# Kernel tuning notes

Hardware: AMD Instinct MI355X
Metric: run time of the kernel (lower is better)

Reference implementation:

```python
import jax, jax.numpy as jnp
import numpy as np

NEG_SLOPE = 0.2
K_L = 0.5
K_G = 0.5
TEMP_G = 1e-3


def _leaky(v):
    return jnp.where(v >= 0, v, NEG_SLOPE * v)


def _topk_row_mask(scores, keep):
    # scores: [n, n, h]; torch.topk(dim=0) -> indices [keep, n] per head,
    # then head_mask[indices, :] = 1 selects whole ROWS (any column hit).
    n = scores.shape[0]
    s = jnp.transpose(scores, (1, 2, 0))        # [n_cols, h, n_rows]
    _, idx = jax.lax.top_k(s, keep)             # [n_cols, h, keep]

    def per_head(idx_h):                        # idx_h: [n_cols, keep]
        return jnp.zeros((n,), scores.dtype).at[idx_h.reshape(-1)].set(1.0)

    rows = jax.vmap(per_head, in_axes=1, out_axes=0)(idx)  # [h, n_rows]
    return jnp.transpose(rows)[:, None, :]      # [n_rows, 1, h] broadcast over cols


def setup_inputs() -> dict:
    key = jax.random.key(0)
    ks = jax.random.split(key, 8)
    n, in_f, feat_dim = 1024, 256, 128
    H, F = 4, 64                                # n_heads, n_hidden (out_features=256)
    feats = jax.random.normal(ks[0], (n, feat_dim), dtype=jnp.float32)
    x = jax.random.normal(ks[1], (n, in_f), dtype=jnp.float32)
    adj = jax.random.randint(ks[2], (n, n, 1), 0, 2).astype(jnp.int32)
    sc = 0.05
    W_l = jax.random.normal(ks[3], (in_f, H * F), dtype=jnp.float32) * sc
    W_r = jax.random.normal(ks[4], (in_f, H * F), dtype=jnp.float32) * sc
    attn_w = jax.random.normal(ks[5], (F,), dtype=jnp.float32) * sc
    W_delta = jax.random.normal(ks[6], (2 * F, F), dtype=jnp.float32) * sc
    b_delta = jnp.zeros((F,), dtype=jnp.float32)
    return {"feats": feats, "x": x, "adj": adj, "W_l": W_l, "W_r": W_r,
            "attn_w": attn_w, "W_delta": W_delta, "b_delta": b_delta}


def reference(feats, x, adj, W_l, W_r, attn_w, W_delta, b_delta):
    n = x.shape[0]
    F = attn_w.shape[0]
    H = W_l.shape[1] // F
    g_l = (x @ W_l).reshape(n, H, F)
    g_r = (x @ W_r).reshape(n, H, F)
    # g_sum[i, j] = g_l[j] + g_r[i]  (repeat vs repeat_interleave ordering)
    g_sum = g_r[:, None, :, :] + g_l[None, :, :, :]          # [n, n, H, F]
    e = jnp.einsum('ijhf,f->ijh', _leaky(g_sum), attn_w)     # [n, n, H]

    mask_adj = adj > 0                                        # [n, n, 1]
    a_l = jax.nn.softmax(jnp.where(mask_adj, e, -jnp.inf), axis=1)
    a_1nd = a_l * mask_adj.astype(e.dtype)

    keep_l = int(n * (1.0 - K_L))
    a_filt = a_1nd * _topk_row_mask(a_1nd, keep_l)
    attn_local = jnp.einsum('ijh,jhf->ihf', a_filt, g_r)     # [n, H, F]

    omega = jax.nn.softmax(e, axis=1)
    fn = (feats - feats.min(axis=0)) / (feats.max(axis=0) - feats.min(axis=0))
    fn = jnp.where(jnp.isnan(fn), 0.0, fn)
    g_rn = (g_r - g_r.min(axis=0)) / (g_r.max(axis=0) - g_r.min(axis=0))
    nf = jnp.linalg.norm(fn, axis=1)                          # [n] (index j)
    ng = jnp.linalg.norm(g_rn, axis=2)                        # [n, H] (index i)
    alpha = jax.nn.softmax(jnp.abs(nf[None, :, None] - ng[:, None, :]), axis=1)
    gamma = 0.5 * (omega + (1.0 - alpha))

    keep_g = int(n * (1.0 - K_G))
    gf = gamma * _topk_row_mask(gamma, keep_g)
    gf = jax.nn.softmax(jnp.where(gf == 0, 1e-10, gf) / TEMP_G, axis=1)
    attn_global = jnp.einsum('ijh,jhf->ihf', gf, g_r)         # [n, H, F]

    inter = _leaky(jnp.concatenate([attn_local, attn_global], axis=2) @ W_delta + b_delta)
    delta = jax.nn.softmax(inter, axis=1)                     # softmax over heads (torch dim=1)
    attn_res = delta * attn_local + (1.0 - delta) * attn_global
    return attn_res.reshape(n, H * F)
```

## Files before the change

kernel.cpp:

```cpp
#include <hip/hip_runtime.h>
#include <cstdint>
#include <cstddef>

#define N 1024
#define HN 4
#define FDIM 64
#define KSEL 512
#define FLT_MAX_ 3.402823466e+38f

__device__ __forceinline__ float wred_sum(float v){
#pragma unroll
  for(int o=32;o>0;o>>=1) v += __shfl_down(v,o,64);
  return v;
}
__device__ __forceinline__ float bfly_sum(float v){
#pragma unroll
  for(int o=1;o<64;o<<=1) v += __shfl_xor(v,o,64);
  return v;
}
__device__ __forceinline__ float bfly_max(float v){
#pragma unroll
  for(int o=1;o<64;o<<=1) v = fmaxf(v,__shfl_xor(v,o,64));
  return v;
}
__device__ __forceinline__ int bfly_sumi(int v){
#pragma unroll
  for(int o=1;o<64;o<<=1) v += __shfl_xor(v,o,64);
  return v;
}
__device__ __forceinline__ float bred_sum(float v, float* scr){
  int t=threadIdx.x;
  v = wred_sum(v);
  __syncthreads();
  if((t&63)==0) scr[t>>6]=v;
  __syncthreads();
  return (scr[0]+scr[1])+(scr[2]+scr[3]);
}

__global__ __launch_bounds__(256) void stage1(const float* __restrict__ x,
                                              const float* __restrict__ W_l,
                                              const float* __restrict__ W_r,
                                              const int* __restrict__ adj,
                                              float* __restrict__ g_l,
                                              float* __restrict__ g_r,
                                              unsigned* __restrict__ adjbit,
                                              int* __restrict__ masks){
  int bx = blockIdx.x, t = threadIdx.x;
  if(bx < 512){
    const float* __restrict__ W = (bx >= 256) ? W_r : W_l;
    float* __restrict__ g = (bx >= 256) ? g_r : g_l;
    int i0 = (bx & 255)*4;
    float acc[4] = {0.f,0.f,0.f,0.f};
#pragma unroll 8
    for(int k=0;k<256;k++){
      float w = W[(size_t)k*256 + t];
#pragma unroll
      for(int r=0;r<4;r++) acc[r] = fmaf(x[(size_t)(i0+r)*256 + k], w, acc[r]);
    }
#pragma unroll
    for(int r=0;r<4;r++) g[(size_t)(i0+r)*256 + t] = acc[r];
  } else {
    int i = bx - 512, w = t>>6, lane = t&63;
    if(i < 32) masks[i*256 + t] = 0;
#pragma unroll
    for(int it=0; it<4; it++){
      int j = w*256 + it*64 + lane;
      int v = adj[(size_t)i*N + j];
      unsigned long long mb = __ballot(v > 0);
      if(lane == 0){
        adjbit[i*32 + w*8 + it*2]     = (unsigned)mb;
        adjbit[i*32 + w*8 + it*2 + 1] = (unsigned)(mb >> 32);
      }
    }
  }
}

__global__ __launch_bounds__(256) void colmm_part(const float* __restrict__ feats,
                                                  const float* __restrict__ g_r,
                                                  float* __restrict__ pmin_f, float* __restrict__ pmax_f,
                                                  float* __restrict__ pmin_g, float* __restrict__ pmax_g){
  int bx = blockIdx.x, t = threadIdx.x;
  int src = (bx >= 16) ? 1 : 0;
  int chunk = src ? bx-16 : bx;
  int cols = src ? 256 : 128;
  const float* in = src ? g_r : feats;
  if(t < cols){
    float lo = FLT_MAX_, hi = -FLT_MAX_;
    int r0 = chunk*64;
    for(int r=0;r<64;r++){
      float v = in[(size_t)(r0+r)*cols + t];
      lo = fminf(lo,v); hi = fmaxf(hi,v);
    }
    if(src){ pmin_g[chunk*256+t]=lo; pmax_g[chunk*256+t]=hi; }
    else   { pmin_f[chunk*128+t]=lo; pmax_f[chunk*128+t]=hi; }
  }
}

__global__ __launch_bounds__(256) void norms_kernel(const float* __restrict__ feats,
                                                    const float* __restrict__ g_r,
                                                    const float* __restrict__ pmin_f, const float* __restrict__ pmax_f,
                                                    const float* __restrict__ pmin_g, const float* __restrict__ pmax_g,
                                                    float* __restrict__ nf, float* __restrict__ ng){
  __shared__ float scr[4];
  int i = blockIdx.x, z = blockIdx.y, t = threadIdx.x;
  if(z==0){
    float u = 0.f;
    if(t < 128){
      float lo = FLT_MAX_, hi = -FLT_MAX_;
#pragma unroll
      for(int k=0;k<16;k++){
        lo = fminf(lo, pmin_f[k*128+t]);
        hi = fmaxf(hi, pmax_f[k*128+t]);
      }
      float d = hi - lo;
      float v = feats[(size_t)i*128 + t];
      u = (d==0.f) ? 0.f : (v - lo)/d;
    }
    float tot = bred_sum(u*u, scr);
    if(t==0) nf[i] = sqrtf(tot);
  } else {
    int c = t, hh = t>>6;
    float lo = FLT_MAX_, hi = -FLT_MAX_;
#pragma unroll
    for(int k=0;k<16;k++){
      lo = fminf(lo, pmin_g[k*256+c]);
      hi = fmaxf(hi, pmax_g[k*256+c]);
    }
    float d = hi - lo;
    float v = g_r[(size_t)i*256 + c];
    float u = (v - lo)/d;
    float ss = wred_sum(u*u);
    if((t&63)==0) ng[hh*N + i] = sqrtf(ss);
  }
}

__global__ __launch_bounds__(256) void compute_e(const float* __restrict__ g_l,
                                                 const float* __restrict__ g_r,
                                                 const float* __restrict__ attn_w,
                                                 float* __restrict__ e){
  __shared__ __align__(16) float grs[64][68];
  __shared__ __align__(16) float gls[64][68];
  __shared__ __align__(16) float aw[64], aw2[64];
  int h = blockIdx.z, i0 = blockIdx.y*64, j0 = blockIdx.x*64;
  int t = threadIdx.x;
  if(t < 64){ float w = attn_w[t]; aw[t]=w; aw2[t]=0.2f*w; }
#pragma unroll
  for(int k=0;k<16;k++){
    int idx = t + k*256; int r = idx>>6, f = idx&63;
    grs[r][f] = g_r[(size_t)(i0+r)*256 + h*64 + f];
    gls[r][f] = g_l[(size_t)(j0+r)*256 + h*64 + f];
  }
  __syncthreads();
  int tj = t&15, ti = t>>4;
  float acc[4][4];
#pragma unroll
  for(int a=0;a<4;a++)
#pragma unroll
    for(int b=0;b<4;b++) acc[a][b]=0.f;
  for(int fc=0; fc<64; fc+=4){
    float4 wv  = *(float4*)&aw[fc];
    float4 wv2 = *(float4*)&aw2[fc];
    float4 ga4[4], gb4[4];
#pragma unroll
    for(int a=0;a<4;a++) ga4[a] = *(float4*)&grs[ti*4+a][fc];
#pragma unroll
    for(int b=0;b<4;b++) gb4[b] = *(float4*)&gls[tj+16*b][fc];
#pragma unroll
    for(int a=0;a<4;a++)
#pragma unroll
      for(int b=0;b<4;b++){
        float s0 = ga4[a].x + gb4[b].x;
        float s1 = ga4[a].y + gb4[b].y;
        float s2 = ga4[a].z + gb4[b].z;
        float s3 = ga4[a].w + gb4[b].w;
        acc[a][b] = fmaf(s0, (s0>=0.f)?wv.x:wv2.x, acc[a][b]);
        acc[a][b] = fmaf(s1, (s1>=0.f)?wv.y:wv2.y, acc[a][b]);
        acc[a][b] = fmaf(s2, (s2>=0.f)?wv.z:wv2.z, acc[a][b]);
        acc[a][b] = fmaf(s3, (s3>=0.f)?wv.w:wv2.w, acc[a][b]);
      }
  }
#pragma unroll
  for(int a=0;a<4;a++)
#pragma unroll
    for(int b=0;b<4;b++){
      int i = i0 + ti*4 + a, j = j0 + tj + 16*b;
      e[((size_t)h*N + i)*N + j] = acc[a][b];
    }
}

__global__ __launch_bounds__(256) void row_stats(const float* __restrict__ e,
                                                 const unsigned* __restrict__ adjbit,
                                                 const float* __restrict__ nf,
                                                 const float* __restrict__ ng,
                                                 float* __restrict__ mlA, float* __restrict__ islA,
                                                 float* __restrict__ moA, float* __restrict__ isoA,
                                                 float* __restrict__ maA, float* __restrict__ isaA,
                                                 float* __restrict__ mgA, float* __restrict__ sgA){
  int i = blockIdx.x, t = threadIdx.x, h = t>>6, lane = t&63;
  size_t base = ((size_t)h*N + i)*N;
  float er[16], nfr[16];
  unsigned nib[4];
#pragma unroll
  for(int c=0;c<4;c++){
    float4 e4 = *(const float4*)(e  + base + c*256 + lane*4);
    float4 n4 = *(const float4*)(nf + c*256 + lane*4);
    er[c*4+0]=e4.x; er[c*4+1]=e4.y; er[c*4+2]=e4.z; er[c*4+3]=e4.w;
    nfr[c*4+0]=n4.x; nfr[c*4+1]=n4.y; nfr[c*4+2]=n4.z; nfr[c*4+3]=n4.w;
    nib[c] = (adjbit[i*32 + c*8 + (lane>>3)] >> ((lane&7)*4)) & 0xFu;
  }
  float ngv = ng[h*N + i];
  float ml=-FLT_MAX_, mo=-FLT_MAX_, ma=-FLT_MAX_;
#pragma unroll
  for(int c=0;c<4;c++)
#pragma unroll
    for(int k=0;k<4;k++){
      int q = c*4+k;
      float ev = er[q];
      mo = fmaxf(mo, ev);
      if((nib[c]>>k)&1) ml = fmaxf(ml, ev);
      ma = fmaxf(ma, fabsf(nfr[q]-ngv));
    }
  ml = bfly_max(ml); mo = bfly_max(mo); ma = bfly_max(ma);
  float sl=0.f, so=0.f, sa=0.f;
#pragma unroll
  for(int c=0;c<4;c++)
#pragma unroll
    for(int k=0;k<4;k++){
      int q = c*4+k;
      float ev = er[q];
      so += __expf(ev-mo);
      if((nib[c]>>k)&1) sl += __expf(ev-ml);
      sa += __expf(fabsf(nfr[q]-ngv)-ma);
    }
  sl = bfly_sum(sl); so = bfly_sum(so); sa = bfly_sum(sa);
  float isl = 1.f/sl, iso = 1.f/so, isa = 1.f/sa;
  float gg[16];
  float mg = -FLT_MAX_;
#pragma unroll
  for(int q=0;q<16;q++){
    float ev = er[q];
    float omega = __expf(ev-mo)*iso;
    float alpha = __expf(fabsf(nfr[q]-ngv)-ma)*isa;
    float g = 0.5f*(omega + 1.f - alpha);
    gg[q] = g;
    mg = fmaxf(mg, g);
  }
  mg = bfly_max(mg);
  float sg = 0.f;
#pragma unroll
  for(int q=0;q<16;q++) sg += __expf((gg[q]-mg)/1e-3f);
  sg = bfly_sum(sg);
  if(lane==0){
    mlA[h*N+i]=ml; islA[h*N+i]=isl;
    moA[h*N+i]=mo; isoA[h*N+i]=iso;
    maA[h*N+i]=ma; isaA[h*N+i]=isa;
    mgA[h*N+i]=mg; sgA[h*N+i]=sg;
  }
}

__global__ __launch_bounds__(256) void applyT(float* __restrict__ e,
                                              float* __restrict__ gamT,
                                              const unsigned* __restrict__ adjbit,
                                              const float* __restrict__ nf,
                                              const float* __restrict__ mlA, const float* __restrict__ islA,
                                              const float* __restrict__ moA, const float* __restrict__ isoA,
                                              const float* __restrict__ maA, const float* __restrict__ isaA,
                                              const float* __restrict__ ng){
  __shared__ __align__(16) float buf1[64][65];
  __shared__ __align__(16) float buf2[64][65];
  __shared__ __align__(16) float buf3[64][65];
  __shared__ float rml[64], risl[64], rmo[64], riso[64], rma[64], risa[64], rng[64], nfs[64];
  int h = blockIdx.y;
  int pp = blockIdx.x; int a = 0;
  while(pp >= 16 - a){ pp -= 16 - a; a++; }
  int b = a + pp;
  int t = threadIdx.x;
  int rg = t >> 4, c4 = t & 15;

  int i0 = a*64, j0 = b*64;
  if(t < 64){
    int o = h*N + i0 + t;
    rml[t]=mlA[o]; risl[t]=islA[o]; rmo[t]=moA[o]; riso[t]=isoA[o];
    rma[t]=maA[o]; risa[t]=isaA[o]; rng[t]=ng[o]; nfs[t]=nf[j0+t];
  }
  __syncthreads();
  float4 ev[4]; unsigned nb[4];
#pragma unroll
  for(int k=0;k<4;k++){
    int row = rg*4+k;
    ev[k] = *(const float4*)(e + ((size_t)h*N + i0+row)*N + j0 + c4*4);
    nb[k] = (adjbit[(size_t)(i0+row)*32 + (j0>>5) + (c4>>3)] >> ((c4&7)*4)) & 0xFu;
  }
#pragma unroll
  for(int k=0;k<4;k++){
    int row = rg*4+k;
    float ml=rml[row], isl=risl[row], mo=rmo[row], iso=riso[row];
    float ma=rma[row], isa=risa[row], ngv=rng[row];
    float evc[4] = {ev[k].x,ev[k].y,ev[k].z,ev[k].w};
#pragma unroll
    for(int c=0;c<4;c++){
      int j = c4*4+c;
      buf2[j][row] = ((nb[k]>>c)&1) ? __expf(evc[c]-ml)*isl : 0.f;
      float omega = __expf(evc[c]-mo)*iso;
      float alpha = __expf(fabsf(nfs[j]-ngv)-ma)*isa;
      buf1[j][row] = 0.5f*(omega + 1.f - alpha);
    }
  }
  __syncthreads();
#pragma unroll
  for(int k=0;k<4;k++){
    int jr = rg*4+k;
    *(float4*)(gamT + ((size_t)h*N + j0+jr)*N + i0 + c4*4) = *(float4*)&buf1[jr][c4*4];
  }
  if(a == b){
#pragma unroll
    for(int k=0;k<4;k++){
      int jr = rg*4+k;
      *(float4*)(e + ((size_t)h*N + j0+jr)*N + i0 + c4*4) = *(float4*)&buf2[jr][c4*4];
    }
    return;
  }
  int i1 = b*64, j1 = a*64;
  __syncthreads();
  if(t < 64){
    int o = h*N + i1 + t;
    rml[t]=mlA[o]; risl[t]=islA[o]; rmo[t]=moA[o]; riso[t]=isoA[o];
    rma[t]=maA[o]; risa[t]=isaA[o]; rng[t]=ng[o]; nfs[t]=nf[j1+t];
  }
#pragma unroll
  for(int k=0;k<4;k++){
    int row = rg*4+k;
    ev[k] = *(const float4*)(e + ((size_t)h*N + i1+row)*N + j1 + c4*4);
    nb[k] = (adjbit[(size_t)(i1+row)*32 + (j1>>5) + (c4>>3)] >> ((c4&7)*4)) & 0xFu;
  }
  __syncthreads();
#pragma unroll
  for(int k=0;k<4;k++){
    int jr = rg*4+k;
    *(float4*)(e + ((size_t)h*N + i1+jr)*N + j1 + c4*4) = *(float4*)&buf2[jr][c4*4];
  }
#pragma unroll
  for(int k=0;k<4;k++){
    int row = rg*4+k;
    float ml=rml[row], isl=risl[row], mo=rmo[row], iso=riso[row];
    float ma=rma[row], isa=risa[row], ngv=rng[row];
    float evc[4] = {ev[k].x,ev[k].y,ev[k].z,ev[k].w};
#pragma unroll
    for(int c=0;c<4;c++){
      int j = c4*4+c;
      buf3[j][row] = ((nb[k]>>c)&1) ? __expf(evc[c]-ml)*isl : 0.f;
      float omega = __expf(evc[c]-mo)*iso;
      float alpha = __expf(fabsf(nfs[j]-ngv)-ma)*isa;
      buf1[j][row] = 0.5f*(omega + 1.f - alpha);
    }
  }
  __syncthreads();
#pragma unroll
  for(int k=0;k<4;k++){
    int jr = rg*4+k;
    *(float4*)(gamT + ((size_t)h*N + j1+jr)*N + i1 + c4*4) = *(float4*)&buf1[jr][c4*4];
    *(float4*)(e    + ((size_t)h*N + j1+jr)*N + i1 + c4*4) = *(float4*)&buf3[jr][c4*4];
  }
}

__global__ __launch_bounds__(256) void colselect6(const float* __restrict__ a1T,
                                                  const float* __restrict__ gaT,
                                                  int* __restrict__ mask_l,
                                                  int* __restrict__ mask_g){
  __shared__ __align__(16) int hist[4][256];
  int t = threadIdx.x, w = t>>6, lane = t&63;
  int gcol = blockIdx.x*4 + w;
  int z  = gcol >> 12;
  int hj = gcol & 4095;
  int h  = hj >> 10;
  const float* __restrict__ src = (z ? gaT : a1T) + (size_t)hj * (size_t)N;
  int* __restrict__ mask = z ? mask_g : mask_l;
  int* hw = hist[w];

  unsigned ur[16];
#pragma unroll
  for(int c=0;c<4;c++){
    uint4 u4 = ((const uint4*)src)[c*64 + lane];
    ur[c*4+0]=u4.x; ur[c*4+1]=u4.y; ur[c*4+2]=u4.z; ur[c*4+3]=u4.w;
  }
  int np = 0;
#pragma unroll
  for(int q=0;q<16;q++) np += (ur[q] != 0u) ? 1 : 0;
  int cnt_pos = bfly_sumi(np);

  unsigned T; int tneed; int tiecnt = -1;
  if(cnt_pos < KSEL){
    T = 0u; tneed = KSEL - cnt_pos;
  } else {
    unsigned prefix = 0; int kth = KSEL;
#pragma unroll
    for(int b=3;b>=0;b--){
      *(int4*)&hw[lane*4] = make_int4(0,0,0,0);
#pragma unroll
      for(int q=0;q<16;q++){
        unsigned u = ur[q];
        bool act = (b==3) || ((u >> (8*(b+1))) == prefix);
        if(act){
          int bucket = (u >> (8*b)) & 0xFF;
          unsigned long long mball = __ballot(true);
          int lead = __ffsll(mball) - 1;
          int maj = __shfl(bucket, lead, 64);
          if(bucket == maj){
            int cnt = (int)__popcll(__ballot(true));
            if(lane == lead) atomicAdd(&hw[maj], cnt);
          } else {
            atomicAdd(&hw[bucket], 1);
          }
        }
      }
      int4 hv = *(int4*)&hw[lane*4];
      int s = hv.x+hv.y+hv.z+hv.w;
      int P = s;
#pragma unroll
      for(int off=1; off<64; off<<=1){
        int q2 = __shfl_up(P, off, 64);
        if(lane >= off) P += q2;
      }
      int total = __shfl(P, 63, 64);
      int suffChunk  = total - (P - s);
      int suffChunkN = total - P;
      bool cross = (suffChunk >= kth) && (suffChunkN < kth);
      int selb=0, newk=0, tcnt=0;
      if(cross){
        int s3 = suffChunkN + hv.w;
        int s2 = s3 + hv.z;
        int s1 = s2 + hv.y;
        if(s3 >= kth){ selb=4*lane+3; newk = kth - suffChunkN; tcnt=hv.w; }
        else if(s2 >= kth){ selb=4*lane+2; newk = kth - s3; tcnt=hv.z; }
        else if(s1 >= kth){ selb=4*lane+1; newk = kth - s2; tcnt=hv.y; }
        else { selb=4*lane; newk = kth - s1; tcnt=hv.x; }
      }
      unsigned long long cm = __ballot(cross);
      int csrc = __ffsll(cm) - 1;
      selb   = __shfl(selb, csrc, 64);
      kth    = __shfl(newk, csrc, 64);
      tiecnt = __shfl(tcnt, csrc, 64);
      prefix = (prefix << 8) | (unsigned)selb;
    }
    T = prefix; tneed = kth;
  }

  if(tiecnt == tneed){
#pragma unroll
    for(int c=0;c<4;c++)
#pragma unroll
      for(int k2=0;k2<4;k2++){
        int i = c*256 + lane*4 + k2;
        if(ur[c*4+k2] >= T) mask[h*N + i] = 1;
      }
  } else {
    int base = 0;
#pragma unroll
    for(int c=0;c<4;c++){
      int tc=0;
#pragma unroll
      for(int k2=0;k2<4;k2++) tc += (ur[c*4+k2]==T)?1:0;
      int pc = tc;
#pragma unroll
      for(int off=1; off<64; off<<=1){
        int q2 = __shfl_up(pc, off, 64);
        if(lane >= off) pc += q2;
      }
      int ctot = __shfl(pc, 63, 64);
      int run = base + pc - tc;
#pragma unroll
      for(int k2=0;k2<4;k2++){
        int i = c*256 + lane*4 + k2;
        unsigned u = ur[c*4+k2];
        bool sel = (u > T) || (u == T && run < tneed);
        run += (u==T)?1:0;
        if(sel) mask[h*N + i] = 1;
      }
      base += ctot;
    }
  }
}

__global__ __launch_bounds__(256) void attn_mm(const float* __restrict__ a1T,
                                               const float* __restrict__ gaT,
                                               const float* __restrict__ g_r,
                                               const float* __restrict__ mgA,
                                               const float* __restrict__ sgA,
                                               const int* __restrict__ mask_g,
                                               float* __restrict__ partL,
                                               float* __restrict__ partG){
  __shared__ __align__(16) float a_t[32][36];
  __shared__ __align__(16) float p_t[32][36];
  __shared__ __align__(16) float b_s[32][68];
  __shared__ float mgv[32], isgv[32];
  __shared__ int mgf[32];
  int i0 = blockIdx.x*32, h = blockIdx.y, s = blockIdx.z, j0 = s*128;
  int t = threadIdx.x;
  if(t < 32){
    mgv[t]  = mgA[h*N + i0 + t];
    isgv[t] = 1.f / sgA[h*N + i0 + t];
    mgf[t]  = mask_g[h*N + i0 + t];
  }
  __syncthreads();
  int fq = t & 15, iq = t >> 4;
  float4 accL[2], accG[2];
#pragma unroll
  for(int r=0;r<2;r++){ accL[r]=make_float4(0,0,0,0); accG[r]=make_float4(0,0,0,0); }
  for(int sub=0; sub<4; sub++){
    int jb = j0 + sub*32;
    {
      int jj = t>>3, i4 = t&7;
      size_t base = ((size_t)h*N + jb + jj)*N + i0 + i4*4;
      *(float4*)&a_t[jj][i4*4] = *(const float4*)(a1T + base);
      float4 g4 = *(const float4*)(gaT + base);
      int ii = i4*4;
      const float inv = 1.f/1024.f;
      float4 p4;
      p4.x = mgf[ii+0] ? __expf((g4.x - mgv[ii+0])/1e-3f)*isgv[ii+0] : inv;
      p4.y = mgf[ii+1] ? __expf((g4.y - mgv[ii+1])/1e-3f)*isgv[ii+1] : inv;
      p4.z = mgf[ii+2] ? __expf((g4.z - mgv[ii+2])/1e-3f)*isgv[ii+2] : inv;
      p4.w = mgf[ii+3] ? __expf((g4.w - mgv[ii+3])/1e-3f)*isgv[ii+3] : inv;
      *(float4*)&p_t[jj][i4*4] = p4;
#pragma unroll
      for(int k=0;k<2;k++){
        int idx = t + k*256;
        int jb2 = idx>>4, d4 = idx&15;
        *(float4*)&b_s[jb2][d4*4] = *(const float4*)(g_r + (size_t)(jb+jb2)*256 + h*64 + d4*4);
      }
    }
    __syncthreads();
#pragma unroll 8
    for(int j=0;j<32;j++){
      float4 bv = *(float4*)&b_s[j][fq*4];
      float2 av = *(float2*)&a_t[j][iq*2];
      float2 pv = *(float2*)&p_t[j][iq*2];
      accL[0].x = fmaf(av.x, bv.x, accL[0].x); accL[0].y = fmaf(av.x, bv.y, accL[0].y);
      accL[0].z = fmaf(av.x, bv.z, accL[0].z); accL[0].w = fmaf(av.x, bv.w, accL[0].w);
      accL[1].x = fmaf(av.y, bv.x, accL[1].x); accL[1].y = fmaf(av.y, bv.y, accL[1].y);
      accL[1].z = fmaf(av.y, bv.z, accL[1].z); accL[1].w = fmaf(av.y, bv.w, accL[1].w);
      accG[0].x = fmaf(pv.x, bv.x, accG[0].x); accG[0].y = fmaf(pv.x, bv.y, accG[0].y);
      accG[0].z = fmaf(pv.x, bv.z, accG[0].z); accG[0].w = fmaf(pv.x, bv.w, accG[0].w);
      accG[1].x = fmaf(pv.y, bv.x, accG[1].x); accG[1].y = fmaf(pv.y, bv.y, accG[1].y);
      accG[1].z = fmaf(pv.y, bv.z, accG[1].z); accG[1].w = fmaf(pv.y, bv.w, accG[1].w);
    }
    __syncthreads();
  }
#pragma unroll
  for(int r=0;r<2;r++){
    int i = i0 + iq*2 + r;
    size_t o = ((size_t)s*N + i)*256 + h*64 + fq*4;
    *(float4*)&partL[o] = accL[r];
    *(float4*)&partG[o] = accG[r];
  }
}

__global__ __launch_bounds__(256) void epilogue(const float* __restrict__ partL,
                                                const float* __restrict__ partG,
                                                const int* __restrict__ mask_l,
                                                const float* __restrict__ W_delta,
                                                const float* __restrict__ b_delta,
                                                float* __restrict__ out){
  __shared__ float cat[4][128];
  __shared__ float inter_s[4][64];
  int i = blockIdx.x, t = threadIdx.x;
  int h = t>>6, f = t&63;
  float sl = 0.f, sg = 0.f;
#pragma unroll
  for(int s2=0;s2<8;s2++){
    size_t o = ((size_t)s2*N + i)*256 + h*64 + f;
    sl += partL[o];
    sg += partG[o];
  }
  if(!mask_l[h*N + i]) sl = 0.f;
  cat[h][f]      = sl;
  cat[h][64 + f] = sg;
  __syncthreads();
  float d = b_delta[f];
  for(int c=0;c<128;c++) d = fmaf(cat[h][c], W_delta[(size_t)c*64 + f], d);
  d = (d >= 0.f) ? d : 0.2f*d;
  inter_s[h][f] = d;
  __syncthreads();
  float m = inter_s[0][f];
#pragma unroll
  for(int hh=1;hh<4;hh++) m = fmaxf(m, inter_s[hh][f]);
  float ssum = 0.f;
#pragma unroll
  for(int hh=0;hh<4;hh++) ssum += __expf(inter_s[hh][f]-m);
  float delta = __expf(d - m)/ssum;
  out[(size_t)i*256 + h*64 + f] = delta*sl + (1.f - delta)*sg;
}

extern "C" void kernel_launch(void* const* d_in, const int* in_sizes, int n_in,
                              void* d_out, int out_size, void* d_ws, size_t ws_size,
                              hipStream_t stream) {
  const float* feats  = (const float*)d_in[0];
  const float* x      = (const float*)d_in[1];
  const int*   adj    = (const int*)  d_in[2];
  const float* W_l    = (const float*)d_in[3];
  const float* W_r    = (const float*)d_in[4];
  const float* attn_w = (const float*)d_in[5];
  const float* W_delta= (const float*)d_in[6];
  const float* b_delta= (const float*)d_in[7];
  float* out = (float*)d_out;

  float* ws = (float*)d_ws;
  size_t off = 0;
  float* g_l   = ws+off; off += (size_t)N*256;
  float* g_r   = ws+off; off += (size_t)N*256;
  float* e     = ws+off; off += (size_t)HN*N*N;
  float* gam   = ws+off; off += (size_t)HN*N*N;
  float* partL = ws+off; off += (size_t)8*N*256;
  float* partG = ws+off; off += (size_t)8*N*256;
  float* pmin_f= ws+off; off += 16*128;
  float* pmax_f= ws+off; off += 16*128;
  float* pmin_g= ws+off; off += 16*256;
  float* pmax_g= ws+off; off += 16*256;
  float* nf    = ws+off; off += N;
  float* ng    = ws+off; off += (size_t)HN*N;
  float* mlA   = ws+off; off += (size_t)HN*N;
  float* islA  = ws+off; off += (size_t)HN*N;
  float* moA   = ws+off; off += (size_t)HN*N;
  float* isoA  = ws+off; off += (size_t)HN*N;
  float* maA   = ws+off; off += (size_t)HN*N;
  float* isaA  = ws+off; off += (size_t)HN*N;
  float* mgA   = ws+off; off += (size_t)HN*N;
  float* sgA   = ws+off; off += (size_t)HN*N;
  int* mask_l  = (int*)(ws+off); off += (size_t)HN*N;
  int* mask_g  = (int*)(ws+off); off += (size_t)HN*N;
  unsigned* adjbit = (unsigned*)(ws+off); off += (size_t)N*32;

  stage1<<<1536, 256, 0, stream>>>(x, W_l, W_r, adj, g_l, g_r, adjbit, mask_l);

  colmm_part<<<32, 256, 0, stream>>>(feats, g_r, pmin_f, pmax_f, pmin_g, pmax_g);

  norms_kernel<<<dim3(N,2), 256, 0, stream>>>(feats, g_r, pmin_f, pmax_f, pmin_g, pmax_g, nf, ng);

  compute_e<<<dim3(16,16,HN), 256, 0, stream>>>(g_l, g_r, attn_w, e);

  row_stats<<<N, 256, 0, stream>>>(e, adjbit, nf, ng, mlA, islA, moA, isoA, maA, isaA, mgA, sgA);

  applyT<<<dim3(136,HN), 256, 0, stream>>>(e, gam, adjbit, nf, mlA, islA, moA, isoA, maA, isaA, ng);

  colselect6<<<2048, 256, 0, stream>>>(e, gam, mask_l, mask_g);

  attn_mm<<<dim3(32,HN,8), 256, 0, stream>>>(e, gam, g_r, mgA, sgA, mask_g, partL, partG);

  epilogue<<<N, 256, 0, stream>>>(partL, partG, mask_l, W_delta, b_delta, out);
}
```

Before: 203.6 us.

## Fold norm stats into earlier kernels and reduce attention partials with atomics

The feats column min/max now runs as extra blocks of stage1. The g_r row norms are computed inside row_stats, which also zeroes the output accumulators, so the old norms kernel shrinks to a feats-only pass. attn_mm now atomically adds its per-split partials into a single N×256 buffer instead of writing 8 separate slices, and the epilogue reads one value. This cuts workspace traffic and the serial 8-way reduction, at the cost of atomic contention and run-to-run nondeterministic summation order.

```diff
diff --git a/kernel.cpp b/kernel.cpp
--- a/kernel.cpp
+++ b/kernel.cpp
@@ -41,10 +41,13 @@
                                               const float* __restrict__ W_l,
                                               const float* __restrict__ W_r,
                                               const int* __restrict__ adj,
+                                              const float* __restrict__ feats,
                                               float* __restrict__ g_l,
                                               float* __restrict__ g_r,
                                               unsigned* __restrict__ adjbit,
-                                              int* __restrict__ masks){
+                                              int* __restrict__ masks,
+                                              float* __restrict__ pmin_f,
+                                              float* __restrict__ pmax_f){
   int bx = blockIdx.x, t = threadIdx.x;
   if(bx < 512){
     const float* __restrict__ W = (bx >= 256) ? W_r : W_l;
@@ -59,7 +62,7 @@
     }
 #pragma unroll
     for(int r=0;r<4;r++) g[(size_t)(i0+r)*256 + t] = acc[r];
-  } else {
+  } else if(bx < 1536){
     int i = bx - 512, w = t>>6, lane = t&63;
     if(i < 32) masks[i*256 + t] = 0;
 #pragma unroll
@@ -72,66 +75,51 @@
         adjbit[i*32 + w*8 + it*2 + 1] = (unsigned)(mb >> 32);
       }
     }
-  }
-}
-
-__global__ __launch_bounds__(256) void colmm_part(const float* __restrict__ feats,
-                                                  const float* __restrict__ g_r,
-                                                  float* __restrict__ pmin_f, float* __restrict__ pmax_f,
-                                                  float* __restrict__ pmin_g, float* __restrict__ pmax_g){
-  int bx = blockIdx.x, t = threadIdx.x;
-  int src = (bx >= 16) ? 1 : 0;
-  int chunk = src ? bx-16 : bx;
-  int cols = src ? 256 : 128;
-  const float* in = src ? g_r : feats;
-  if(t < cols){
-    float lo = FLT_MAX_, hi = -FLT_MAX_;
-    int r0 = chunk*64;
-    for(int r=0;r<64;r++){
-      float v = in[(size_t)(r0+r)*cols + t];
-      lo = fminf(lo,v); hi = fmaxf(hi,v);
-    }
-    if(src){ pmin_g[chunk*256+t]=lo; pmax_g[chunk*256+t]=hi; }
-    else   { pmin_f[chunk*128+t]=lo; pmax_f[chunk*128+t]=hi; }
-  }
-}
-
-__global__ __launch_bounds__(256) void norms_kernel(const float* __restrict__ feats,
-                                                    const float* __restrict__ g_r,
-                                                    const float* __restrict__ pmin_f, const float* __restrict__ pmax_f,
-                                                    const float* __restrict__ pmin_g, const float* __restrict__ pmax_g,
-                                                    float* __restrict__ nf, float* __restrict__ ng){
-  __shared__ float scr[4];
-  int i = blockIdx.x, z = blockIdx.y, t = threadIdx.x;
-  if(z==0){
-    float u = 0.f;
+  } else {
+    int chunk = bx - 1536;
     if(t < 128){
       float lo = FLT_MAX_, hi = -FLT_MAX_;
-#pragma unroll
-      for(int k=0;k<16;k++){
-        lo = fminf(lo, pmin_f[k*128+t]);
-        hi = fmaxf(hi, pmax_f[k*128+t]);
-      }
-      float d = hi - lo;
-      float v = feats[(size_t)i*128 + t];
-      u = (d==0.f) ? 0.f : (v - lo)/d;
-    }
-    float tot = bred_sum(u*u, scr);
-    if(t==0) nf[i] = sqrtf(tot);
-  } else {
-    int c = t, hh = t>>6;
+      int r0 = chunk*64;
+      for(int r=0;r<64;r++){
+        float v = feats[(size_t)(r0+r)*128 + t];
+        lo = fminf(lo,v); hi = fmaxf(hi,v);
+      }
+      pmin_f[chunk*128+t]=lo; pmax_f[chunk*128+t]=hi;
+    }
+  }
+}
+
+__global__ __launch_bounds__(256) void colmm_part(const float* __restrict__ g_r,
+                                                  float* __restrict__ pmin_g, float* __restrict__ pmax_g){
+  int chunk = blockIdx.x, t = threadIdx.x;
+  float lo = FLT_MAX_, hi = -FLT_MAX_;
+  int r0 = chunk*64;
+  for(int r=0;r<64;r++){
+    float v = g_r[(size_t)(r0+r)*256 + t];
+    lo = fminf(lo,v); hi = fmaxf(hi,v);
+  }
+  pmin_g[chunk*256+t]=lo; pmax_g[chunk*256+t]=hi;
+}
+
+__global__ __launch_bounds__(256) void norms_nf(const float* __restrict__ feats,
+                                                const float* __restrict__ pmin_f, const float* __restrict__ pmax_f,
+                                                float* __restrict__ nf){
+  __shared__ float scr[4];
+  int i = blockIdx.x, t = threadIdx.x;
+  float u = 0.f;
+  if(t < 128){
     float lo = FLT_MAX_, hi = -FLT_MAX_;
 #pragma unroll
     for(int k=0;k<16;k++){
-      lo = fminf(lo, pmin_g[k*256+c]);
-      hi = fmaxf(hi, pmax_g[k*256+c]);
+      lo = fminf(lo, pmin_f[k*128+t]);
+      hi = fmaxf(hi, pmax_f[k*128+t]);
     }
     float d = hi - lo;
-    float v = g_r[(size_t)i*256 + c];
-    float u = (v - lo)/d;
-    float ss = wred_sum(u*u);
-    if((t&63)==0) ng[hh*N + i] = sqrtf(ss);
-  }
+    float v = feats[(size_t)i*128 + t];
+    u = (d==0.f) ? 0.f : (v - lo)/d;
+  }
+  float tot = bred_sum(u*u, scr);
+  if(t==0) nf[i] = sqrtf(tot);
 }
 
 __global__ __launch_bounds__(256) void compute_e(const float* __restrict__ g_l,
@@ -191,12 +179,27 @@
 __global__ __launch_bounds__(256) void row_stats(const float* __restrict__ e,
                                                  const unsigned* __restrict__ adjbit,
                                                  const float* __restrict__ nf,
-                                                 const float* __restrict__ ng,
+                                                 const float* __restrict__ g_r,
+                                                 const float* __restrict__ pmin_g, const float* __restrict__ pmax_g,
+                                                 float* __restrict__ ng,
                                                  float* __restrict__ mlA, float* __restrict__ islA,
                                                  float* __restrict__ moA, float* __restrict__ isoA,
                                                  float* __restrict__ maA, float* __restrict__ isaA,
-                                                 float* __restrict__ mgA, float* __restrict__ sgA){
+                                                 float* __restrict__ mgA, float* __restrict__ sgA,
+                                                 float* __restrict__ partLG){
   int i = blockIdx.x, t = threadIdx.x, h = t>>6, lane = t&63;
+  ((float2*)partLG)[(size_t)i*256 + t] = make_float2(0.f, 0.f);
+  float glo = FLT_MAX_, ghi = -FLT_MAX_;
+#pragma unroll
+  for(int k=0;k<16;k++){
+    glo = fminf(glo, pmin_g[k*256 + h*64 + lane]);
+    ghi = fmaxf(ghi, pmax_g[k*256 + h*64 + lane]);
+  }
+  float dg = ghi - glo;
+  float ug = (g_r[(size_t)i*256 + h*64 + lane] - glo)/dg;
+  float ngv = sqrtf(bfly_sum(ug*ug));
+  if(lane==0) ng[h*N + i] = ngv;
+
   size_t base = ((size_t)h*N + i)*N;
   float er[16], nfr[16];
   unsigned nib[4];
@@ -208,7 +211,6 @@
     nfr[c*4+0]=n4.x; nfr[c*4+1]=n4.y; nfr[c*4+2]=n4.z; nfr[c*4+3]=n4.w;
     nib[c] = (adjbit[i*32 + c*8 + (lane>>3)] >> ((lane&7)*4)) & 0xFu;
   }
-  float ngv = ng[h*N + i];
   float ml=-FLT_MAX_, mo=-FLT_MAX_, ma=-FLT_MAX_;
 #pragma unroll
   for(int c=0;c<4;c++)
@@ -548,9 +550,11 @@
 #pragma unroll
   for(int r=0;r<2;r++){
     int i = i0 + iq*2 + r;
-    size_t o = ((size_t)s*N + i)*256 + h*64 + fq*4;
-    *(float4*)&partL[o] = accL[r];
-    *(float4*)&partG[o] = accG[r];
+    size_t o = (size_t)i*256 + h*64 + fq*4;
+    atomicAdd(&partL[o+0], accL[r].x); atomicAdd(&partL[o+1], accL[r].y);
+    atomicAdd(&partL[o+2], accL[r].z); atomicAdd(&partL[o+3], accL[r].w);
+    atomicAdd(&partG[o+0], accG[r].x); atomicAdd(&partG[o+1], accG[r].y);
+    atomicAdd(&partG[o+2], accG[r].z); atomicAdd(&partG[o+3], accG[r].w);
   }
 }
 
@@ -564,13 +568,9 @@
   __shared__ float inter_s[4][64];
   int i = blockIdx.x, t = threadIdx.x;
   int h = t>>6, f = t&63;
-  float sl = 0.f, sg = 0.f;
-#pragma unroll
-  for(int s2=0;s2<8;s2++){
-    size_t o = ((size_t)s2*N + i)*256 + h*64 + f;
-    sl += partL[o];
-    sg += partG[o];
-  }
+  size_t o = (size_t)i*256 + h*64 + f;
+  float sl = partL[o];
+  float sg = partG[o];
   if(!mask_l[h*N + i]) sl = 0.f;
   cat[h][f]      = sl;
   cat[h][64 + f] = sg;
@@ -609,8 +609,8 @@
   float* g_r   = ws+off; off += (size_t)N*256;
   float* e     = ws+off; off += (size_t)HN*N*N;
   float* gam   = ws+off; off += (size_t)HN*N*N;
-  float* partL = ws+off; off += (size_t)8*N*256;
-  float* partG = ws+off; off += (size_t)8*N*256;
+  float* partL = ws+off; off += (size_t)N*256;
+  float* partG = ws+off; off += (size_t)N*256;
   float* pmin_f= ws+off; off += 16*128;
   float* pmax_f= ws+off; off += 16*128;
   float* pmin_g= ws+off; off += 16*256;
@@ -629,15 +629,16 @@
   int* mask_g  = (int*)(ws+off); off += (size_t)HN*N;
   unsigned* adjbit = (unsigned*)(ws+off); off += (size_t)N*32;
 
-  stage1<<<1536, 256, 0, stream>>>(x, W_l, W_r, adj, g_l, g_r, adjbit, mask_l);
-
-  colmm_part<<<32, 256, 0, stream>>>(feats, g_r, pmin_f, pmax_f, pmin_g, pmax_g);
-
-  norms_kernel<<<dim3(N,2), 256, 0, stream>>>(feats, g_r, pmin_f, pmax_f, pmin_g, pmax_g, nf, ng);
+  stage1<<<1552, 256, 0, stream>>>(x, W_l, W_r, adj, feats, g_l, g_r, adjbit, mask_l, pmin_f, pmax_f);
+
+  colmm_part<<<16, 256, 0, stream>>>(g_r, pmin_g, pmax_g);
+
+  norms_nf<<<N, 256, 0, stream>>>(feats, pmin_f, pmax_f, nf);
 
   compute_e<<<dim3(16,16,HN), 256, 0, stream>>>(g_l, g_r, attn_w, e);
 
-  row_stats<<<N, 256, 0, stream>>>(e, adjbit, nf, ng, mlA, islA, moA, isoA, maA, isaA, mgA, sgA);
+  row_stats<<<N, 256, 0, stream>>>(e, adjbit, nf, g_r, pmin_g, pmax_g, ng,
+                                   mlA, islA, moA, isoA, maA, isaA, mgA, sgA, partL);
 
   applyT<<<dim3(136,HN), 256, 0, stream>>>(e, gam, adjbit, nf, mlA, islA, moA, isoA, maA, isaA, ng);
 
```

After: 242.5 us. 1.19x slower.
